# Performance work log

Measured on AMD Instinct MI355X. Metric: run time of the kernel, lower is better.

## Reference

```python
import jax, jax.numpy as jnp
import numpy as np

B, N, E, H, EF = 4, 10000, 160000, 128, 32

def dense(x, w, b):
    # Dense = Linear + SiLU activation
    return jax.nn.silu(x @ w + b)

def residual(x, w, b):
    # Residual(mlp_num=2): x + Dense(Dense(x))
    return x + dense(dense(x, w[0], b[0]), w[1], b[1])

def setup_inputs() -> dict:
    key = jax.random.key(0)
    ks = jax.random.split(key, 8)
    s = 0.05
    return dict(
        scalar=jax.random.normal(ks[0], (B, N, H), jnp.float32),
        ef=jax.random.normal(ks[1], (B, E, EF), jnp.float32),
        edge_index=jax.random.randint(ks[2], (B, E, 2), 0, N),
        C=jax.random.uniform(ks[3], (B, 1, 1), jnp.float32),
        emb_w=jax.random.normal(ks[4], (2, 2, H, H), jnp.float32) * s,
        emb_b=jnp.zeros((2, 2, H), jnp.float32),
        e_w=jax.random.normal(ks[5], (EF, H), jnp.float32) * s,
        conv_w=jax.random.normal(ks[6], (2, 2, H, H), jnp.float32) * s,
        conv_b=jnp.zeros((2, 2, H), jnp.float32),
        out_w=jax.random.normal(ks[7], (2, H, H), jnp.float32) * s,
        out_b=jnp.zeros((2, H), jnp.float32),
    )

def reference(scalar, ef, edge_index, C, emb_w, emb_b, e_w, conv_w, conv_b, out_w, out_b):
    row = edge_index[..., 0]   # [B,E] destination (scatter) indices
    col = edge_index[..., 1]   # [B,E] source (gather) indices
    # two 2-layer Dense MLPs on node features
    s2s = dense(dense(scalar, emb_w[0, 0], emb_b[0, 0]), emb_w[0, 1], emb_b[0, 1])       # [B,N,H]
    scalar_dst = dense(dense(scalar, emb_w[1, 0], emb_b[1, 0]), emb_w[1, 1], emb_b[1, 1])  # [B,N,H]
    ef_proj = ef @ e_w                                                                   # [B,E,H]
    # gather node feats at col, multiply by edge projection
    scalar_edge = jnp.take_along_axis(scalar_dst, col[..., None], axis=1) * ef_proj      # [B,E,H]
    # scatter-sum by row per batch element
    conv = jax.vmap(lambda x, r: jax.ops.segment_sum(x, r, num_segments=N))(scalar_edge, row)  # [B,N,H]
    conv = conv * C
    conv = residual(conv, conv_w[0], conv_b[0])
    conv = residual(conv, conv_w[1], conv_b[1])
    out = residual(s2s * conv, out_w, out_b)
    return out
```

## Files before the change

### kernel.cpp

```cpp
#include <hip/hip_runtime.h>
#include <hip/hip_bf16.h>

#define H 128
#define CAP 48
#define CSTRIDE 16

typedef _Float16 f16x4 __attribute__((ext_vector_type(4)));
typedef _Float16 f16x8 __attribute__((ext_vector_type(8)));
typedef float    f32x4 __attribute__((ext_vector_type(4)));
typedef float    f32x2 __attribute__((ext_vector_type(2)));

__device__ __forceinline__ float silu_f(float v) {
    return v / (1.0f + __expf(-v));
}

__global__ __launch_bounds__(256)
void pack_w(const float* __restrict__ emb_w, const float* __restrict__ conv_w,
            const float* __restrict__ out_w, const float* __restrict__ e_w,
            _Float16* __restrict__ wpk, int* __restrict__ cnt)
{
    const int gid = blockIdx.x * 256 + threadIdx.x;

#pragma unroll
    for (int i = 0; i < 32; ++i) {
        const int idx = gid + i * 20992;
        if (idx < 40960 * CSTRIDE) cnt[idx] = 0;
    }

    _Float16* dst = wpk + (size_t)gid * 8;
    if (gid < 20480) {
        const int mat = gid >> 11;
        const int r   = gid & 2047;
        const int ct  = r >> 8;
        const int kb  = (r >> 6) & 3;
        const int lane = r & 63;
        const float* W = (mat < 4) ? emb_w + mat * 16384
                       : (mat < 8) ? conv_w + (mat - 4) * 16384
                                   : out_w + (mat - 8) * 16384;
        const int m  = ct * 16 + (lane & 15);
        const int k0 = kb * 32 + (lane >> 4) * 8;
#pragma unroll
        for (int j = 0; j < 8; ++j)
            dst[j] = (_Float16)W[(k0 + j) * H + m];
    } else {
        const int r    = gid - 20480;
        const int ct   = r >> 6;
        const int lane = r & 63;
        const int m    = ct * 16 + (lane & 15);
        const int k0   = (lane >> 4) * 8;
#pragma unroll
        for (int j = 0; j < 8; ++j)
            dst[j] = (_Float16)e_w[(k0 + j) * H + m];
    }
}

template <int CT>
__device__ __forceinline__ void mfma_layerT(const _Float16* __restrict__ w,
                                            const f16x8 bf[4], int ct0, int lane,
                                            f32x4 acc[CT])
{
#pragma unroll
    for (int c = 0; c < CT; ++c) acc[c] = (f32x4){0.f, 0.f, 0.f, 0.f};
#pragma unroll
    for (int kb = 0; kb < 4; ++kb) {
#pragma unroll
        for (int ctl = 0; ctl < CT; ++ctl) {
            f16x8 af = *(const f16x8*)(w + ((size_t)((ct0 + ctl) * 4 + kb) * 64 + lane) * 8);
            acc[ctl] = __builtin_amdgcn_mfma_f32_16x16x32_f16(af, bf[kb], acc[ctl], 0, 0, 0);
        }
    }
}

template <int CT>
__device__ __forceinline__ void store_stripT(_Float16* strip, const f32x4 acc[CT],
                                             const float* bias, int ct0, int rl, int quad)
{
#pragma unroll
    for (int ctl = 0; ctl < CT; ++ctl) {
        const int c = (ct0 + ctl) * 16 + quad * 4;
        float4 bb = *(const float4*)(bias + c);
        f16x4 hv = {(_Float16)silu_f(acc[ctl][0] + bb.x),
                    (_Float16)silu_f(acc[ctl][1] + bb.y),
                    (_Float16)silu_f(acc[ctl][2] + bb.z),
                    (_Float16)silu_f(acc[ctl][3] + bb.w)};
        *(f16x4*)(strip + rl * 136 + c) = hv;
    }
}

template <int CT>
__device__ __forceinline__ void store_strip_rawT(_Float16* strip, const f32x4 t[CT],
                                                 int ct0, int rl, int quad)
{
#pragma unroll
    for (int ctl = 0; ctl < CT; ++ctl) {
        const int c = (ct0 + ctl) * 16 + quad * 4;
        f16x4 hv = {(_Float16)t[ctl][0], (_Float16)t[ctl][1],
                    (_Float16)t[ctl][2], (_Float16)t[ctl][3]};
        *(f16x4*)(strip + rl * 136 + c) = hv;
    }
}

__device__ __forceinline__ void load_bf(const _Float16* strip, f16x8 bf[4],
                                        int rl, int quad)
{
#pragma unroll
    for (int kb = 0; kb < 4; ++kb)
        bf[kb] = *(const f16x8*)(strip + rl * 136 + kb * 32 + quad * 8);
}

__global__ __launch_bounds__(256)
void embscat_k(const float* __restrict__ x, const _Float16* __restrict__ wpk,
               const float* __restrict__ emb_b,
               float* __restrict__ s2s, float* __restrict__ sdst,
               const int* __restrict__ eidx, int* __restrict__ cnt,
               int2* __restrict__ bucket)
{
    __shared__ _Float16 hsA[16 * 136], hsB[16 * 136];

    if (blockIdx.x < 2500) {
        const int e = blockIdx.x * 256 + threadIdx.x;
        const int2 rc = ((const int2*)eidx)[e];
        const int b = (unsigned)e / 160000u;
        const int key = b * 10000 + rc.x;
        const int pos = atomicAdd(&cnt[key * CSTRIDE], 1);
        if (pos < CAP)
            bucket[(size_t)key * CAP + pos] = make_int2(e, b * 10000 + rc.y);
        return;
    }

    const int bid  = blockIdx.x - 2500;
    const int tid  = threadIdx.x;
    const int lane = tid & 63;
    const int wid  = tid >> 6;
    const int half = wid & 1;
    const int msel = wid >> 1;
    const int rl   = lane & 15;
    const int quad = lane >> 4;
    const int row  = bid * 16 + rl;
    const size_t rbase = (size_t)row * H;

    f16x8 bf[4];
#pragma unroll
    for (int kb = 0; kb < 4; ++kb) {
        const int kc = kb * 32 + quad * 8;
        float4 v0 = *(const float4*)(x + rbase + kc);
        float4 v1 = *(const float4*)(x + rbase + kc + 4);
        bf[kb] = (f16x8){(_Float16)v0.x, (_Float16)v0.y, (_Float16)v0.z, (_Float16)v0.w,
                         (_Float16)v1.x, (_Float16)v1.y, (_Float16)v1.z, (_Float16)v1.w};
    }

    const _Float16* wm = wpk + (size_t)msel * 2 * 16384;
    _Float16* strip = msel ? hsB : hsA;
    const float* bias0 = emb_b + msel * 2 * H;

    f32x4 acc[4];
    mfma_layerT<4>(wm, bf, half * 4, lane, acc);
    store_stripT<4>(strip, acc, bias0, half * 4, rl, quad);
    __syncthreads();
    load_bf(strip, bf, rl, quad);
    mfma_layerT<4>(wm + 16384, bf, half * 4, lane, acc);

    float* outp = msel ? sdst : s2s;
    const float* bias1 = bias0 + H;
#pragma unroll
    for (int ctl = 0; ctl < 4; ++ctl) {
        const int c = (half * 4 + ctl) * 16 + quad * 4;
        float4 bb = *(const float4*)(bias1 + c);
        float4 v;
        v.x = silu_f(acc[ctl][0] + bb.x);
        v.y = silu_f(acc[ctl][1] + bb.y);
        v.z = silu_f(acc[ctl][2] + bb.z);
        v.w = silu_f(acc[ctl][3] + bb.w);
        *(float4*)(outp + rbase + c) = v;
    }
}

__global__ __launch_bounds__(256)
void out6_k(const float* __restrict__ conv, const float* __restrict__ s2s,
            const _Float16* __restrict__ w6,
            const float* __restrict__ conv_b, const float* __restrict__ out_b,
            float* __restrict__ y)
{
    __shared__ _Float16 hs0[16 * 136], hs1[16 * 136];
    const int tid  = threadIdx.x;
    const int lane = tid & 63;
    const int ct0  = (tid >> 6) * 2;
    const int rl   = lane & 15;
    const int quad = lane >> 4;
    const int row  = blockIdx.x * 16 + rl;
    const size_t rbase = (size_t)row * H;

    f16x8 bf[4];
#pragma unroll
    for (int kb = 0; kb < 4; ++kb) {
        const int kc = kb * 32 + quad * 8;
        float4 v0 = *(const float4*)(conv + rbase + kc);
        float4 v1 = *(const float4*)(conv + rbase + kc + 4);
        bf[kb] = (f16x8){(_Float16)v0.x, (_Float16)v0.y, (_Float16)v0.z, (_Float16)v0.w,
                         (_Float16)v1.x, (_Float16)v1.y, (_Float16)v1.z, (_Float16)v1.w};
    }

    f32x4 acc[2], tD[2];

    mfma_layerT<2>(w6, bf, ct0, lane, acc);
    store_stripT<2>(hs0, acc, conv_b, ct0, rl, quad);
    __syncthreads();
    load_bf(hs0, bf, rl, quad);

    mfma_layerT<2>(w6 + 16384, bf, ct0, lane, acc);
#pragma unroll
    for (int ctl = 0; ctl < 2; ++ctl) {
        const int c = (ct0 + ctl) * 16 + quad * 4;
        float4 bb = *(const float4*)(conv_b + H + c);
        float4 cv = *(const float4*)(conv + rbase + c);
        tD[ctl][0] = cv.x + silu_f(acc[ctl][0] + bb.x);
        tD[ctl][1] = cv.y + silu_f(acc[ctl][1] + bb.y);
        tD[ctl][2] = cv.z + silu_f(acc[ctl][2] + bb.z);
        tD[ctl][3] = cv.w + silu_f(acc[ctl][3] + bb.w);
    }
    store_strip_rawT<2>(hs1, tD, ct0, rl, quad);
    __syncthreads();
    load_bf(hs1, bf, rl, quad);

    mfma_layerT<2>(w6 + 2 * 16384, bf, ct0, lane, acc);
    store_stripT<2>(hs0, acc, conv_b + 2 * H, ct0, rl, quad);
    __syncthreads();
    load_bf(hs0, bf, rl, quad);

    mfma_layerT<2>(w6 + 3 * 16384, bf, ct0, lane, acc);
#pragma unroll
    for (int ctl = 0; ctl < 2; ++ctl) {
        const int c = (ct0 + ctl) * 16 + quad * 4;
        float4 bb = *(const float4*)(conv_b + 3 * H + c);
        float4 sv = *(const float4*)(s2s + rbase + c);
        tD[ctl][0] = (tD[ctl][0] + silu_f(acc[ctl][0] + bb.x)) * sv.x;
        tD[ctl][1] = (tD[ctl][1] + silu_f(acc[ctl][1] + bb.y)) * sv.y;
        tD[ctl][2] = (tD[ctl][2] + silu_f(acc[ctl][2] + bb.z)) * sv.z;
        tD[ctl][3] = (tD[ctl][3] + silu_f(acc[ctl][3] + bb.w)) * sv.w;
    }
    store_strip_rawT<2>(hs1, tD, ct0, rl, quad);
    __syncthreads();
    load_bf(hs1, bf, rl, quad);

    mfma_layerT<2>(w6 + 4 * 16384, bf, ct0, lane, acc);
    store_stripT<2>(hs0, acc, out_b, ct0, rl, quad);
    __syncthreads();
    load_bf(hs0, bf, rl, quad);

    mfma_layerT<2>(w6 + 5 * 16384, bf, ct0, lane, acc);
#pragma unroll
    for (int ctl = 0; ctl < 2; ++ctl) {
        const int c = (ct0 + ctl) * 16 + quad * 4;
        float4 bb = *(const float4*)(out_b + H + c);
        float4 v;
        v.x = tD[ctl][0] + silu_f(acc[ctl][0] + bb.x);
        v.y = tD[ctl][1] + silu_f(acc[ctl][1] + bb.y);
        v.z = tD[ctl][2] + silu_f(acc[ctl][2] + bb.z);
        v.w = tD[ctl][3] + silu_f(acc[ctl][3] + bb.w);
        *(float4*)(y + rbase + c) = v;
    }
}

#define GLD(dst, p, offlit) \
    asm volatile("global_load_dword %0, %1, off offset:" offlit \
                 : "=v"(dst) : "v"(p))
#define GLDX4(dst, p, offlit) \
    asm volatile("global_load_dwordx4 %0, %1, off offset:" offlit \
                 : "=v"(dst) : "v"(p))

__global__ __launch_bounds__(256, 2)
void conv_k(const float* __restrict__ ef, const float* __restrict__ sdst,
            const _Float16* __restrict__ ewpk, const float* __restrict__ C,
            const int* __restrict__ cnt, const int2* __restrict__ bucket,
            float* __restrict__ conv)
{
    const int tid  = threadIdx.x;
    const int lane = tid & 63;
    const int el   = lane & 15;
    const int quad = lane >> 4;
    const int nid  = blockIdx.x * 4 + (tid >> 6);

    const int n = min(cnt[nid * CSTRIDE], CAP);
    const int2* bk = bucket + (size_t)nid * CAP;

    f16x8 bw[8];
#pragma unroll
    for (int ct = 0; ct < 8; ++ct)
        bw[ct] = *(const f16x8*)(ewpk + ((size_t)((ct << 6) + lane)) * 8);

    float part[8];
#pragma unroll
    for (int ct = 0; ct < 8; ++ct) part[ct] = 0.f;

#pragma unroll 1
    for (int base = 0; base < n; base += 16) {
        const int rem = n - base;
        const bool ok = (el < rem);
        int2 md = make_int2(0, 0);
        if (ok) md = bk[base + el];

        const int sc0 = __shfl(md.y, (quad << 2) | 0, 64);
        const int sc1 = __shfl(md.y, (quad << 2) | 1, 64);
        const int sc2 = __shfl(md.y, (quad << 2) | 2, 64);
        const int sc3 = __shfl(md.y, (quad << 2) | 3, 64);

        const float* pe = ef + (size_t)md.x * 32 + (quad << 3);
        const float* p0 = sdst + (size_t)sc0 * H + el;
        const float* p1 = sdst + (size_t)sc1 * H + el;
        const float* p2 = sdst + (size_t)sc2 * H + el;
        const float* p3 = sdst + (size_t)sc3 * H + el;

        f32x4 v0, v1;
        GLDX4(v0, pe, "0");
        GLDX4(v1, pe, "16");
        float s0[8], s1[8], s2[8], s3[8];
        GLD(s0[0], p0, "0");   GLD(s0[1], p0, "64");  GLD(s0[2], p0, "128");
        GLD(s0[3], p0, "192"); GLD(s0[4], p0, "256"); GLD(s0[5], p0, "320");
        GLD(s0[6], p0, "384"); GLD(s0[7], p0, "448");
        GLD(s1[0], p1, "0");   GLD(s1[1], p1, "64");  GLD(s1[2], p1, "128");
        GLD(s1[3], p1, "192"); GLD(s1[4], p1, "256"); GLD(s1[5], p1, "320");
        GLD(s1[6], p1, "384"); GLD(s1[7], p1, "448");
        GLD(s2[0], p2, "0");   GLD(s2[1], p2, "64");  GLD(s2[2], p2, "128");
        GLD(s2[3], p2, "192"); GLD(s2[4], p2, "256"); GLD(s2[5], p2, "320");
        GLD(s2[6], p2, "384"); GLD(s2[7], p2, "448");
        GLD(s3[0], p3, "0");   GLD(s3[1], p3, "64");  GLD(s3[2], p3, "128");
        GLD(s3[3], p3, "192"); GLD(s3[4], p3, "256"); GLD(s3[5], p3, "320");
        GLD(s3[6], p3, "384"); GLD(s3[7], p3, "448");

        asm volatile("s_waitcnt vmcnt(0)" ::: "memory");
        __builtin_amdgcn_sched_barrier(0);

        const f16x8 af = {
            ok ? (_Float16)v0[0] : (_Float16)0.f, ok ? (_Float16)v0[1] : (_Float16)0.f,
            ok ? (_Float16)v0[2] : (_Float16)0.f, ok ? (_Float16)v0[3] : (_Float16)0.f,
            ok ? (_Float16)v1[0] : (_Float16)0.f, ok ? (_Float16)v1[1] : (_Float16)0.f,
            ok ? (_Float16)v1[2] : (_Float16)0.f, ok ? (_Float16)v1[3] : (_Float16)0.f};

#pragma unroll
        for (int ct = 0; ct < 8; ++ct) {
            f32x4 acc = __builtin_amdgcn_mfma_f32_16x16x32_f16(
                af, bw[ct], (f32x4){0.f, 0.f, 0.f, 0.f}, 0, 0, 0);
            part[ct] += acc[0] * s0[ct] + acc[1] * s1[ct]
                      + acc[2] * s2[ct] + acc[3] * s3[ct];
        }
    }

    const float Cb = C[(unsigned)nid / 10000u];
    float w0 = 0.f, w1 = 0.f;
#pragma unroll
    for (int ct = 0; ct < 8; ++ct) {
        float v = part[ct];
        v += __shfl_xor(v, 16, 64);
        v += __shfl_xor(v, 32, 64);
        v *= Cb;
        if ((ct >> 1) == quad) { if (ct & 1) w1 = v; else w0 = v; }
    }
    float* dst = conv + (size_t)nid * H + (quad << 5) + el;
    dst[0]  = w0;
    dst[16] = w1;
}

extern "C" void kernel_launch(void* const* d_in, const int* in_sizes, int n_in,
                              void* d_out, int out_size, void* d_ws, size_t ws_size,
                              hipStream_t stream)
{
    const float* scalar = (const float*)d_in[0];
    const float* ef     = (const float*)d_in[1];
    const int*   eidx   = (const int*)d_in[2];
    const float* C      = (const float*)d_in[3];
    const float* emb_w  = (const float*)d_in[4];
    const float* emb_b  = (const float*)d_in[5];
    const float* e_w    = (const float*)d_in[6];
    const float* conv_w = (const float*)d_in[7];
    const float* conv_b = (const float*)d_in[8];
    const float* out_w  = (const float*)d_in[9];
    const float* out_b  = (const float*)d_in[10];

    const int M = 40000;
    const size_t nodeElems = (size_t)M * H;

    float* s2s  = (float*)d_ws;
    float* sdst = s2s + nodeElems;
    float* conv = sdst + nodeElems;
    _Float16* wpk = (_Float16*)(conv + nodeElems);
    int* cnt    = (int*)(wpk + 167936);
    int2* bucket = (int2*)(cnt + 40960 * CSTRIDE);

    dim3 blk(256);

    pack_w<<<82, blk, 0, stream>>>(emb_w, conv_w, out_w, e_w, wpk, cnt);
    embscat_k<<<5000, blk, 0, stream>>>(scalar, wpk, emb_b, s2s, sdst,
                                        eidx, cnt, bucket);
    conv_k<<<10000, blk, 0, stream>>>(ef, sdst, wpk + 163840, C, cnt, bucket, conv);
    out6_k<<<2500, blk, 0, stream>>>(conv, s2s, wpk + 4 * 16384,
                                     conv_b, out_b, (float*)d_out);
}
```

Baseline: 310.0 us.

## Process two nodes per wave in conv kernel with packed 32-bit bucket entries

```diff
diff --git a/kernel.cpp b/kernel.cpp
--- a/kernel.cpp
+++ b/kernel.cpp
@@ -113,22 +113,23 @@
                const float* __restrict__ emb_b,
                float* __restrict__ s2s, float* __restrict__ sdst,
                const int* __restrict__ eidx, int* __restrict__ cnt,
-               int2* __restrict__ bucket)
+               unsigned* __restrict__ bucket)
 {
     __shared__ _Float16 hsA[16 * 136], hsB[16 * 136];
 
-    if (blockIdx.x < 2500) {
-        const int e = blockIdx.x * 256 + threadIdx.x;
+    if (blockIdx.x & 1) {
+        const int e = (blockIdx.x >> 1) * 256 + threadIdx.x;
         const int2 rc = ((const int2*)eidx)[e];
         const int b = (unsigned)e / 160000u;
         const int key = b * 10000 + rc.x;
         const int pos = atomicAdd(&cnt[key * CSTRIDE], 1);
         if (pos < CAP)
-            bucket[(size_t)key * CAP + pos] = make_int2(e, b * 10000 + rc.y);
+            bucket[(size_t)key * CAP + pos] =
+                ((unsigned)(e - b * 160000) << 14) | (unsigned)rc.y;
         return;
     }
 
-    const int bid  = blockIdx.x - 2500;
+    const int bid  = blockIdx.x >> 1;
     const int tid  = threadIdx.x;
     const int lane = tid & 63;
     const int wid  = tid >> 6;
@@ -268,96 +269,175 @@
     asm volatile("global_load_dwordx4 %0, %1, off offset:" offlit \
                  : "=v"(dst) : "v"(p))
 
-__global__ __launch_bounds__(256, 2)
+__device__ __forceinline__ void tile_pair(
+    const float* __restrict__ ef, const float* __restrict__ sdst,
+    const f16x8 bw[8], unsigned mA, unsigned mB,
+    int ebase, int srow, int quad, int el, bool okA, bool okB,
+    float pA[8], float pB[8])
+{
+    const int scA0 = srow + (__shfl((int)mA, (quad << 2) | 0, 64) & 0x3FFF);
+    const int scA1 = srow + (__shfl((int)mA, (quad << 2) | 1, 64) & 0x3FFF);
+    const int scA2 = srow + (__shfl((int)mA, (quad << 2) | 2, 64) & 0x3FFF);
+    const int scA3 = srow + (__shfl((int)mA, (quad << 2) | 3, 64) & 0x3FFF);
+    const int scB0 = srow + (__shfl((int)mB, (quad << 2) | 0, 64) & 0x3FFF);
+    const int scB1 = srow + (__shfl((int)mB, (quad << 2) | 1, 64) & 0x3FFF);
+    const int scB2 = srow + (__shfl((int)mB, (quad << 2) | 2, 64) & 0x3FFF);
+    const int scB3 = srow + (__shfl((int)mB, (quad << 2) | 3, 64) & 0x3FFF);
+
+    const float* peA = ef + (size_t)(ebase + (int)(mA >> 14)) * 32 + (quad << 3);
+    const float* peB = ef + (size_t)(ebase + (int)(mB >> 14)) * 32 + (quad << 3);
+    const float* a0 = sdst + (size_t)scA0 * H + el;
+    const float* a1 = sdst + (size_t)scA1 * H + el;
+    const float* a2 = sdst + (size_t)scA2 * H + el;
+    const float* a3 = sdst + (size_t)scA3 * H + el;
+    const float* b0 = sdst + (size_t)scB0 * H + el;
+    const float* b1 = sdst + (size_t)scB1 * H + el;
+    const float* b2 = sdst + (size_t)scB2 * H + el;
+    const float* b3 = sdst + (size_t)scB3 * H + el;
+
+    f32x4 vA0, vA1, vB0, vB1;
+    float sA0[8], sA1[8], sA2[8], sA3[8];
+    float sB0[8], sB1[8], sB2[8], sB3[8];
+
+    GLDX4(vA0, peA, "0");
+    GLDX4(vA1, peA, "16");
+    GLD(sA0[0], a0, "0");   GLD(sA0[1], a0, "64");  GLD(sA0[2], a0, "128");
+    GLD(sA0[3], a0, "192"); GLD(sA0[4], a0, "256"); GLD(sA0[5], a0, "320");
+    GLD(sA0[6], a0, "384"); GLD(sA0[7], a0, "448");
+    GLD(sA1[0], a1, "0");   GLD(sA1[1], a1, "64");  GLD(sA1[2], a1, "128");
+    GLD(sA1[3], a1, "192"); GLD(sA1[4], a1, "256"); GLD(sA1[5], a1, "320");
+    GLD(sA1[6], a1, "384"); GLD(sA1[7], a1, "448");
+    GLD(sA2[0], a2, "0");   GLD(sA2[1], a2, "64");  GLD(sA2[2], a2, "128");
+    GLD(sA2[3], a2, "192"); GLD(sA2[4], a2, "256"); GLD(sA2[5], a2, "320");
+    GLD(sA2[6], a2, "384"); GLD(sA2[7], a2, "448");
+    GLD(sA3[0], a3, "0");   GLD(sA3[1], a3, "64");  GLD(sA3[2], a3, "128");
+    GLD(sA3[3], a3, "192"); GLD(sA3[4], a3, "256"); GLD(sA3[5], a3, "320");
+    GLD(sA3[6], a3, "384"); GLD(sA3[7], a3, "448");
+
+    GLDX4(vB0, peB, "0");
+    GLDX4(vB1, peB, "16");
+    GLD(sB0[0], b0, "0");   GLD(sB0[1], b0, "64");  GLD(sB0[2], b0, "128");
+    GLD(sB0[3], b0, "192"); GLD(sB0[4], b0, "256"); GLD(sB0[5], b0, "320");
+    GLD(sB0[6], b0, "384"); GLD(sB0[7], b0, "448");
+    GLD(sB1[0], b1, "0");   GLD(sB1[1], b1, "64");  GLD(sB1[2], b1, "128");
+    GLD(sB1[3], b1, "192"); GLD(sB1[4], b1, "256"); GLD(sB1[5], b1, "320");
+    GLD(sB1[6], b1, "384"); GLD(sB1[7], b1, "448");
+    GLD(sB2[0], b2, "0");   GLD(sB2[1], b2, "64");  GLD(sB2[2], b2, "128");
+    GLD(sB2[3], b2, "192"); GLD(sB2[4], b2, "256"); GLD(sB2[5], b2, "320");
+    GLD(sB2[6], b2, "384"); GLD(sB2[7], b2, "448");
+    GLD(sB3[0], b3, "0");   GLD(sB3[1], b3, "64");  GLD(sB3[2], b3, "128");
+    GLD(sB3[3], b3, "192"); GLD(sB3[4], b3, "256"); GLD(sB3[5], b3, "320");
+    GLD(sB3[6], b3, "384"); GLD(sB3[7], b3, "448");
+
+    asm volatile("s_waitcnt vmcnt(34)" ::: "memory");
+    __builtin_amdgcn_sched_barrier(0);
+
+    const f16x8 afA = {
+        okA ? (_Float16)vA0[0] : (_Float16)0.f, okA ? (_Float16)vA0[1] : (_Float16)0.f,
+        okA ? (_Float16)vA0[2] : (_Float16)0.f, okA ? (_Float16)vA0[3] : (_Float16)0.f,
+        okA ? (_Float16)vA1[0] : (_Float16)0.f, okA ? (_Float16)vA1[1] : (_Float16)0.f,
+        okA ? (_Float16)vA1[2] : (_Float16)0.f, okA ? (_Float16)vA1[3] : (_Float16)0.f};
+#pragma unroll
+    for (int ct = 0; ct < 8; ++ct) {
+        f32x4 acc = __builtin_amdgcn_mfma_f32_16x16x32_f16(
+            afA, bw[ct], (f32x4){0.f, 0.f, 0.f, 0.f}, 0, 0, 0);
+        pA[ct] += acc[0] * sA0[ct] + acc[1] * sA1[ct]
+                + acc[2] * sA2[ct] + acc[3] * sA3[ct];
+    }
+
+    __builtin_amdgcn_sched_barrier(0);
+    asm volatile("s_waitcnt vmcnt(0)" ::: "memory");
+    __builtin_amdgcn_sched_barrier(0);
+
+    const f16x8 afB = {
+        okB ? (_Float16)vB0[0] : (_Float16)0.f, okB ? (_Float16)vB0[1] : (_Float16)0.f,
+        okB ? (_Float16)vB0[2] : (_Float16)0.f, okB ? (_Float16)vB0[3] : (_Float16)0.f,
+        okB ? (_Float16)vB1[0] : (_Float16)0.f, okB ? (_Float16)vB1[1] : (_Float16)0.f,
+        okB ? (_Float16)vB1[2] : (_Float16)0.f, okB ? (_Float16)vB1[3] : (_Float16)0.f};
+#pragma unroll
+    for (int ct = 0; ct < 8; ++ct) {
+        f32x4 acc = __builtin_amdgcn_mfma_f32_16x16x32_f16(
+            afB, bw[ct], (f32x4){0.f, 0.f, 0.f, 0.f}, 0, 0, 0);
+        pB[ct] += acc[0] * sB0[ct] + acc[1] * sB1[ct]
+                + acc[2] * sB2[ct] + acc[3] * sB3[ct];
+    }
+}
+
+__global__ __launch_bounds__(256)
 void conv_k(const float* __restrict__ ef, const float* __restrict__ sdst,
             const _Float16* __restrict__ ewpk, const float* __restrict__ C,
-            const int* __restrict__ cnt, const int2* __restrict__ bucket,
+            const int* __restrict__ cnt, const unsigned* __restrict__ bucket,
             float* __restrict__ conv)
 {
     const int tid  = threadIdx.x;
     const int lane = tid & 63;
     const int el   = lane & 15;
     const int quad = lane >> 4;
-    const int nid  = blockIdx.x * 4 + (tid >> 6);
-
-    const int n = min(cnt[nid * CSTRIDE], CAP);
-    const int2* bk = bucket + (size_t)nid * CAP;
+    const int p    = blockIdx.x * 4 + (tid >> 6);
+    const int nA   = 2 * p, nB = nA + 1;
+    const int b    = (unsigned)nA / 10000u;
+    const int ebase = b * 160000;
+    const int srow  = b * 10000;
+
+    const unsigned* bkA = bucket + (size_t)nA * CAP;
+    const unsigned* bkB = bucket + (size_t)nB * CAP;
+
+    const unsigned eA0 = bkA[el], eA1 = bkA[16 + el];
+    const unsigned eB0 = bkB[el], eB1 = bkB[16 + el];
+    const int cA = min(cnt[nA * CSTRIDE], CAP);
+    const int cB = min(cnt[nB * CSTRIDE], CAP);
+    const int nmax = max(cA, cB);
 
     f16x8 bw[8];
 #pragma unroll
     for (int ct = 0; ct < 8; ++ct)
         bw[ct] = *(const f16x8*)(ewpk + ((size_t)((ct << 6) + lane)) * 8);
 
-    float part[8];
-#pragma unroll
-    for (int ct = 0; ct < 8; ++ct) part[ct] = 0.f;
-
+    float pA[8], pB[8];
+#pragma unroll
+    for (int ct = 0; ct < 8; ++ct) { pA[ct] = 0.f; pB[ct] = 0.f; }
+
+    {
+        const bool okA = el < cA, okB = el < cB;
+        tile_pair(ef, sdst, bw, okA ? eA0 : 0u, okB ? eB0 : 0u,
+                  ebase, srow, quad, el, okA, okB, pA, pB);
+    }
+    if (nmax > 16) {
+        const bool okA = el < cA - 16, okB = el < cB - 16;
+        tile_pair(ef, sdst, bw, okA ? eA1 : 0u, okB ? eB1 : 0u,
+                  ebase, srow, quad, el, okA, okB, pA, pB);
+    }
 #pragma unroll 1
-    for (int base = 0; base < n; base += 16) {
-        const int rem = n - base;
-        const bool ok = (el < rem);
-        int2 md = make_int2(0, 0);
-        if (ok) md = bk[base + el];
-
-        const int sc0 = __shfl(md.y, (quad << 2) | 0, 64);
-        const int sc1 = __shfl(md.y, (quad << 2) | 1, 64);
-        const int sc2 = __shfl(md.y, (quad << 2) | 2, 64);
-        const int sc3 = __shfl(md.y, (quad << 2) | 3, 64);
-
-        const float* pe = ef + (size_t)md.x * 32 + (quad << 3);
-        const float* p0 = sdst + (size_t)sc0 * H + el;
-        const float* p1 = sdst + (size_t)sc1 * H + el;
-        const float* p2 = sdst + (size_t)sc2 * H + el;
-        const float* p3 = sdst + (size_t)sc3 * H + el;
-
-        f32x4 v0, v1;
-        GLDX4(v0, pe, "0");
-        GLDX4(v1, pe, "16");
-        float s0[8], s1[8], s2[8], s3[8];
-        GLD(s0[0], p0, "0");   GLD(s0[1], p0, "64");  GLD(s0[2], p0, "128");
-        GLD(s0[3], p0, "192"); GLD(s0[4], p0, "256"); GLD(s0[5], p0, "320");
-        GLD(s0[6], p0, "384"); GLD(s0[7], p0, "448");
-        GLD(s1[0], p1, "0");   GLD(s1[1], p1, "64");  GLD(s1[2], p1, "128");
-        GLD(s1[3], p1, "192"); GLD(s1[4], p1, "256"); GLD(s1[5], p1, "320");
-        GLD(s1[6], p1, "384"); GLD(s1[7], p1, "448");
-        GLD(s2[0], p2, "0");   GLD(s2[1], p2, "64");  GLD(s2[2], p2, "128");
-        GLD(s2[3], p2, "192"); GLD(s2[4], p2, "256"); GLD(s2[5], p2, "320");
-        GLD(s2[6], p2, "384"); GLD(s2[7], p2, "448");
-        GLD(s3[0], p3, "0");   GLD(s3[1], p3, "64");  GLD(s3[2], p3, "128");
-        GLD(s3[3], p3, "192"); GLD(s3[4], p3, "256"); GLD(s3[5], p3, "320");
-        GLD(s3[6], p3, "384"); GLD(s3[7], p3, "448");
-
-        asm volatile("s_waitcnt vmcnt(0)" ::: "memory");
-        __builtin_amdgcn_sched_barrier(0);
-
-        const f16x8 af = {
-            ok ? (_Float16)v0[0] : (_Float16)0.f, ok ? (_Float16)v0[1] : (_Float16)0.f,
-            ok ? (_Float16)v0[2] : (_Float16)0.f, ok ? (_Float16)v0[3] : (_Float16)0.f,
-            ok ? (_Float16)v1[0] : (_Float16)0.f, ok ? (_Float16)v1[1] : (_Float16)0.f,
-            ok ? (_Float16)v1[2] : (_Float16)0.f, ok ? (_Float16)v1[3] : (_Float16)0.f};
-
-#pragma unroll
-        for (int ct = 0; ct < 8; ++ct) {
-            f32x4 acc = __builtin_amdgcn_mfma_f32_16x16x32_f16(
-                af, bw[ct], (f32x4){0.f, 0.f, 0.f, 0.f}, 0, 0, 0);
-            part[ct] += acc[0] * s0[ct] + acc[1] * s1[ct]
-                      + acc[2] * s2[ct] + acc[3] * s3[ct];
+    for (int base = 32; base < nmax; base += 16) {
+        const bool okA = el < cA - base, okB = el < cB - base;
+        const unsigned tA = okA ? bkA[base + el] : 0u;
+        const unsigned tB = okB ? bkB[base + el] : 0u;
+        tile_pair(ef, sdst, bw, tA, tB, ebase, srow, quad, el, okA, okB, pA, pB);
+    }
+
+    const float Cb = C[b];
+    float w0A = 0.f, w1A = 0.f, w0B = 0.f, w1B = 0.f;
+#pragma unroll
+    for (int ct = 0; ct < 8; ++ct) {
+        float vA = pA[ct];
+        vA += __shfl_xor(vA, 16, 64);
+        vA += __shfl_xor(vA, 32, 64);
+        vA *= Cb;
+        float vB = pB[ct];
+        vB += __shfl_xor(vB, 16, 64);
+        vB += __shfl_xor(vB, 32, 64);
+        vB *= Cb;
+        if ((ct >> 1) == quad) {
+            if (ct & 1) { w1A = vA; w1B = vB; }
+            else        { w0A = vA; w0B = vB; }
         }
     }
-
-    const float Cb = C[(unsigned)nid / 10000u];
-    float w0 = 0.f, w1 = 0.f;
-#pragma unroll
-    for (int ct = 0; ct < 8; ++ct) {
-        float v = part[ct];
-        v += __shfl_xor(v, 16, 64);
-        v += __shfl_xor(v, 32, 64);
-        v *= Cb;
-        if ((ct >> 1) == quad) { if (ct & 1) w1 = v; else w0 = v; }
-    }
-    float* dst = conv + (size_t)nid * H + (quad << 5) + el;
-    dst[0]  = w0;
-    dst[16] = w1;
+    float* dstA = conv + (size_t)nA * H + (quad << 5) + el;
+    dstA[0]  = w0A;
+    dstA[16] = w1A;
+    float* dstB = conv + (size_t)nB * H + (quad << 5) + el;
+    dstB[0]  = w0B;
+    dstB[16] = w1B;
 }
 
 extern "C" void kernel_launch(void* const* d_in, const int* in_sizes, int n_in,
@@ -384,14 +464,14 @@
     float* conv = sdst + nodeElems;
     _Float16* wpk = (_Float16*)(conv + nodeElems);
     int* cnt    = (int*)(wpk + 167936);
-    int2* bucket = (int2*)(cnt + 40960 * CSTRIDE);
+    unsigned* bucket = (unsigned*)(cnt + 40960 * CSTRIDE);
 
     dim3 blk(256);
 
     pack_w<<<82, blk, 0, stream>>>(emb_w, conv_w, out_w, e_w, wpk, cnt);
     embscat_k<<<5000, blk, 0, stream>>>(scalar, wpk, emb_b, s2s, sdst,
                                         eidx, cnt, bucket);
-    conv_k<<<10000, blk, 0, stream>>>(ef, sdst, wpk + 163840, C, cnt, bucket, conv);
+    conv_k<<<5000, blk, 0, stream>>>(ef, sdst, wpk + 163840, C, cnt, bucket, conv);
     out6_k<<<2500, blk, 0, stream>>>(conv, s2s, wpk + 4 * 16384,
                                      conv_b, out_b, (float*)d_out);
 }
```

Result: slower. 319.3 us (+3.0%).

## Give each wave full-width MLP rows, pack bucket entries, interleave scatter blocks

Applied to the files above, without the earlier changes.

```diff
diff --git a/kernel.cpp b/kernel.cpp
--- a/kernel.cpp
+++ b/kernel.cpp
@@ -8,7 +8,6 @@
 typedef _Float16 f16x4 __attribute__((ext_vector_type(4)));
 typedef _Float16 f16x8 __attribute__((ext_vector_type(8)));
 typedef float    f32x4 __attribute__((ext_vector_type(4)));
-typedef float    f32x2 __attribute__((ext_vector_type(2)));
 
 __device__ __forceinline__ float silu_f(float v) {
     return v / (1.0f + __expf(-v));
@@ -113,30 +112,34 @@
                const float* __restrict__ emb_b,
                float* __restrict__ s2s, float* __restrict__ sdst,
                const int* __restrict__ eidx, int* __restrict__ cnt,
-               int2* __restrict__ bucket)
-{
-    __shared__ _Float16 hsA[16 * 136], hsB[16 * 136];
-
-    if (blockIdx.x < 2500) {
-        const int e = blockIdx.x * 256 + threadIdx.x;
+               unsigned* __restrict__ bucket, const float* __restrict__ ef)
+{
+    __shared__ _Float16 hs[4][16 * 136];
+    const int g = blockIdx.x / 3, r = blockIdx.x % 3;
+
+    if (r < 2) {
+        const int e = (g * 2 + r) * 256 + threadIdx.x;
         const int2 rc = ((const int2*)eidx)[e];
         const int b = (unsigned)e / 160000u;
         const int key = b * 10000 + rc.x;
         const int pos = atomicAdd(&cnt[key * CSTRIDE], 1);
         if (pos < CAP)
-            bucket[(size_t)key * CAP + pos] = make_int2(e, b * 10000 + rc.y);
+            bucket[(size_t)key * CAP + pos] =
+                ((unsigned)(e - b * 160000) << 14) | (unsigned)rc.y;
+        const float w0 = ef[(size_t)e * 32];
+        const float w1 = ef[(size_t)e * 32 + 16];
+        asm volatile("" :: "v"(w0), "v"(w1));
         return;
     }
 
-    const int bid  = blockIdx.x - 2500;
     const int tid  = threadIdx.x;
     const int lane = tid & 63;
     const int wid  = tid >> 6;
-    const int half = wid & 1;
-    const int msel = wid >> 1;
+    const int msel = wid & 1;
+    const int rg   = wid >> 1;
     const int rl   = lane & 15;
     const int quad = lane >> 4;
-    const int row  = bid * 16 + rl;
+    const int row  = g * 32 + rg * 16 + rl;
     const size_t rbase = (size_t)row * H;
 
     f16x8 bf[4];
@@ -150,21 +153,21 @@
     }
 
     const _Float16* wm = wpk + (size_t)msel * 2 * 16384;
-    _Float16* strip = msel ? hsB : hsA;
+    _Float16* strip = hs[wid];
     const float* bias0 = emb_b + msel * 2 * H;
 
-    f32x4 acc[4];
-    mfma_layerT<4>(wm, bf, half * 4, lane, acc);
-    store_stripT<4>(strip, acc, bias0, half * 4, rl, quad);
-    __syncthreads();
-    load_bf(strip, bf, rl, quad);
-    mfma_layerT<4>(wm + 16384, bf, half * 4, lane, acc);
+    f32x4 acc[8];
+    mfma_layerT<8>(wm, bf, 0, lane, acc);
+    store_stripT<8>(strip, acc, bias0, 0, rl, quad);
+    __builtin_amdgcn_sched_barrier(0);
+    load_bf(strip, bf, rl, quad);
+    mfma_layerT<8>(wm + 16384, bf, 0, lane, acc);
 
     float* outp = msel ? sdst : s2s;
     const float* bias1 = bias0 + H;
 #pragma unroll
-    for (int ctl = 0; ctl < 4; ++ctl) {
-        const int c = (half * 4 + ctl) * 16 + quad * 4;
+    for (int ctl = 0; ctl < 8; ++ctl) {
+        const int c = ctl * 16 + quad * 4;
         float4 bb = *(const float4*)(bias1 + c);
         float4 v;
         v.x = silu_f(acc[ctl][0] + bb.x);
@@ -181,14 +184,15 @@
             const float* __restrict__ conv_b, const float* __restrict__ out_b,
             float* __restrict__ y)
 {
-    __shared__ _Float16 hs0[16 * 136], hs1[16 * 136];
+    __shared__ _Float16 hs[4][16 * 136];
     const int tid  = threadIdx.x;
     const int lane = tid & 63;
-    const int ct0  = (tid >> 6) * 2;
+    const int wid  = tid >> 6;
     const int rl   = lane & 15;
     const int quad = lane >> 4;
-    const int row  = blockIdx.x * 16 + rl;
+    const int row  = blockIdx.x * 64 + wid * 16 + rl;
     const size_t rbase = (size_t)row * H;
+    _Float16* strip = hs[wid];
 
     f16x8 bf[4];
 #pragma unroll
@@ -200,17 +204,17 @@
                          (_Float16)v1.x, (_Float16)v1.y, (_Float16)v1.z, (_Float16)v1.w};
     }
 
-    f32x4 acc[2], tD[2];
-
-    mfma_layerT<2>(w6, bf, ct0, lane, acc);
-    store_stripT<2>(hs0, acc, conv_b, ct0, rl, quad);
-    __syncthreads();
-    load_bf(hs0, bf, rl, quad);
-
-    mfma_layerT<2>(w6 + 16384, bf, ct0, lane, acc);
-#pragma unroll
-    for (int ctl = 0; ctl < 2; ++ctl) {
-        const int c = (ct0 + ctl) * 16 + quad * 4;
+    f32x4 acc[8], tD[8];
+
+    mfma_layerT<8>(w6, bf, 0, lane, acc);
+    store_stripT<8>(strip, acc, conv_b, 0, rl, quad);
+    __builtin_amdgcn_sched_barrier(0);
+    load_bf(strip, bf, rl, quad);
+
+    mfma_layerT<8>(w6 + 16384, bf, 0, lane, acc);
+#pragma unroll
+    for (int ctl = 0; ctl < 8; ++ctl) {
+        const int c = ctl * 16 + quad * 4;
         float4 bb = *(const float4*)(conv_b + H + c);
         float4 cv = *(const float4*)(conv + rbase + c);
         tD[ctl][0] = cv.x + silu_f(acc[ctl][0] + bb.x);
@@ -218,19 +222,19 @@
         tD[ctl][2] = cv.z + silu_f(acc[ctl][2] + bb.z);
         tD[ctl][3] = cv.w + silu_f(acc[ctl][3] + bb.w);
     }
-    store_strip_rawT<2>(hs1, tD, ct0, rl, quad);
-    __syncthreads();
-    load_bf(hs1, bf, rl, quad);
-
-    mfma_layerT<2>(w6 + 2 * 16384, bf, ct0, lane, acc);
-    store_stripT<2>(hs0, acc, conv_b + 2 * H, ct0, rl, quad);
-    __syncthreads();
-    load_bf(hs0, bf, rl, quad);
-
-    mfma_layerT<2>(w6 + 3 * 16384, bf, ct0, lane, acc);
-#pragma unroll
-    for (int ctl = 0; ctl < 2; ++ctl) {
-        const int c = (ct0 + ctl) * 16 + quad * 4;
+    store_strip_rawT<8>(strip, tD, 0, rl, quad);
+    __builtin_amdgcn_sched_barrier(0);
+    load_bf(strip, bf, rl, quad);
+
+    mfma_layerT<8>(w6 + 2 * 16384, bf, 0, lane, acc);
+    store_stripT<8>(strip, acc, conv_b + 2 * H, 0, rl, quad);
+    __builtin_amdgcn_sched_barrier(0);
+    load_bf(strip, bf, rl, quad);
+
+    mfma_layerT<8>(w6 + 3 * 16384, bf, 0, lane, acc);
+#pragma unroll
+    for (int ctl = 0; ctl < 8; ++ctl) {
+        const int c = ctl * 16 + quad * 4;
         float4 bb = *(const float4*)(conv_b + 3 * H + c);
         float4 sv = *(const float4*)(s2s + rbase + c);
         tD[ctl][0] = (tD[ctl][0] + silu_f(acc[ctl][0] + bb.x)) * sv.x;
@@ -238,19 +242,19 @@
         tD[ctl][2] = (tD[ctl][2] + silu_f(acc[ctl][2] + bb.z)) * sv.z;
         tD[ctl][3] = (tD[ctl][3] + silu_f(acc[ctl][3] + bb.w)) * sv.w;
     }
-    store_strip_rawT<2>(hs1, tD, ct0, rl, quad);
-    __syncthreads();
-    load_bf(hs1, bf, rl, quad);
-
-    mfma_layerT<2>(w6 + 4 * 16384, bf, ct0, lane, acc);
-    store_stripT<2>(hs0, acc, out_b, ct0, rl, quad);
-    __syncthreads();
-    load_bf(hs0, bf, rl, quad);
-
-    mfma_layerT<2>(w6 + 5 * 16384, bf, ct0, lane, acc);
-#pragma unroll
-    for (int ctl = 0; ctl < 2; ++ctl) {
-        const int c = (ct0 + ctl) * 16 + quad * 4;
+    store_strip_rawT<8>(strip, tD, 0, rl, quad);
+    __builtin_amdgcn_sched_barrier(0);
+    load_bf(strip, bf, rl, quad);
+
+    mfma_layerT<8>(w6 + 4 * 16384, bf, 0, lane, acc);
+    store_stripT<8>(strip, acc, out_b, 0, rl, quad);
+    __builtin_amdgcn_sched_barrier(0);
+    load_bf(strip, bf, rl, quad);
+
+    mfma_layerT<8>(w6 + 5 * 16384, bf, 0, lane, acc);
+#pragma unroll
+    for (int ctl = 0; ctl < 8; ++ctl) {
+        const int c = ctl * 16 + quad * 4;
         float4 bb = *(const float4*)(out_b + H + c);
         float4 v;
         v.x = tD[ctl][0] + silu_f(acc[ctl][0] + bb.x);
@@ -271,7 +275,7 @@
 __global__ __launch_bounds__(256, 2)
 void conv_k(const float* __restrict__ ef, const float* __restrict__ sdst,
             const _Float16* __restrict__ ewpk, const float* __restrict__ C,
-            const int* __restrict__ cnt, const int2* __restrict__ bucket,
+            const int* __restrict__ cnt, const unsigned* __restrict__ bucket,
             float* __restrict__ conv)
 {
     const int tid  = threadIdx.x;
@@ -279,9 +283,12 @@
     const int el   = lane & 15;
     const int quad = lane >> 4;
     const int nid  = blockIdx.x * 4 + (tid >> 6);
+    const int b    = (unsigned)nid / 10000u;
+    const int ebase = b * 160000;
+    const int srow  = b * 10000;
 
     const int n = min(cnt[nid * CSTRIDE], CAP);
-    const int2* bk = bucket + (size_t)nid * CAP;
+    const unsigned* bk = bucket + (size_t)nid * CAP;
 
     f16x8 bw[8];
 #pragma unroll
@@ -296,15 +303,14 @@
     for (int base = 0; base < n; base += 16) {
         const int rem = n - base;
         const bool ok = (el < rem);
-        int2 md = make_int2(0, 0);
-        if (ok) md = bk[base + el];
-
-        const int sc0 = __shfl(md.y, (quad << 2) | 0, 64);
-        const int sc1 = __shfl(md.y, (quad << 2) | 1, 64);
-        const int sc2 = __shfl(md.y, (quad << 2) | 2, 64);
-        const int sc3 = __shfl(md.y, (quad << 2) | 3, 64);
-
-        const float* pe = ef + (size_t)md.x * 32 + (quad << 3);
+        const unsigned m = ok ? bk[base + el] : 0u;
+
+        const int sc0 = srow + (__shfl((int)m, (quad << 2) | 0, 64) & 0x3FFF);
+        const int sc1 = srow + (__shfl((int)m, (quad << 2) | 1, 64) & 0x3FFF);
+        const int sc2 = srow + (__shfl((int)m, (quad << 2) | 2, 64) & 0x3FFF);
+        const int sc3 = srow + (__shfl((int)m, (quad << 2) | 3, 64) & 0x3FFF);
+
+        const float* pe = ef + (size_t)(ebase + (int)(m >> 14)) * 32 + (quad << 3);
         const float* p0 = sdst + (size_t)sc0 * H + el;
         const float* p1 = sdst + (size_t)sc1 * H + el;
         const float* p2 = sdst + (size_t)sc2 * H + el;
@@ -345,7 +351,7 @@
         }
     }
 
-    const float Cb = C[(unsigned)nid / 10000u];
+    const float Cb = C[b];
     float w0 = 0.f, w1 = 0.f;
 #pragma unroll
     for (int ct = 0; ct < 8; ++ct) {
@@ -384,14 +390,14 @@
     float* conv = sdst + nodeElems;
     _Float16* wpk = (_Float16*)(conv + nodeElems);
     int* cnt    = (int*)(wpk + 167936);
-    int2* bucket = (int2*)(cnt + 40960 * CSTRIDE);
+    unsigned* bucket = (unsigned*)(cnt + 40960 * CSTRIDE);
 
     dim3 blk(256);
 
     pack_w<<<82, blk, 0, stream>>>(emb_w, conv_w, out_w, e_w, wpk, cnt);
-    embscat_k<<<5000, blk, 0, stream>>>(scalar, wpk, emb_b, s2s, sdst,
-                                        eidx, cnt, bucket);
+    embscat_k<<<3750, blk, 0, stream>>>(scalar, wpk, emb_b, s2s, sdst,
+                                        eidx, cnt, bucket, ef);
     conv_k<<<10000, blk, 0, stream>>>(ef, sdst, wpk + 163840, C, cnt, bucket, conv);
-    out6_k<<<2500, blk, 0, stream>>>(conv, s2s, wpk + 4 * 16384,
-                                     conv_b, out_b, (float*)d_out);
-}
+    out6_k<<<625, blk, 0, stream>>>(conv, s2s, wpk + 4 * 16384,
+                                    conv_b, out_b, (float*)d_out);
+}
```

Measured after the change: 303.1 us. -2.2%, faster.
